# Kernel tuning notes

Measured on AMD Instinct MI355X. Metric: run time of the kernel, lower is better.

Reference implementation:

```python
import jax, jax.numpy as jnp
import numpy as np

D = 1024
DFF = 4096
B, S = 4, 2048
EPS = 1e-6
SLOPE = 0.01  # torch LeakyReLU default


def setup_inputs() -> dict:
    key = jax.random.key(0)
    ks = jax.random.split(key, 16)
    sd = 1.0 / np.sqrt(D)
    sf = 1.0 / np.sqrt(DFF)
    return {
        "X": jax.random.normal(ks[0], (B, S, D), dtype=jnp.float32),
        "intensity": jax.random.uniform(ks[1], (B, S, S), dtype=jnp.float32),
        "Wq": jax.random.uniform(ks[2], (D, D), jnp.float32, -sd, sd),
        "bq": jax.random.uniform(ks[3], (D,), jnp.float32, -sd, sd),
        "Wk": jax.random.uniform(ks[4], (D, D), jnp.float32, -sd, sd),
        "bk": jax.random.uniform(ks[5], (D,), jnp.float32, -sd, sd),
        "Wv": jax.random.uniform(ks[6], (D, D), jnp.float32, -sd, sd),
        "bv": jax.random.uniform(ks[7], (D,), jnp.float32, -sd, sd),
        "Wo": jax.random.uniform(ks[8], (D, D), jnp.float32, -sd, sd),
        "bo": jax.random.uniform(ks[9], (D,), jnp.float32, -sd, sd),
        "W1": jax.random.uniform(ks[10], (D, DFF), jnp.float32, -sd, sd),
        "b1": jax.random.uniform(ks[11], (DFF,), jnp.float32, -sd, sd),
        "W2": jax.random.uniform(ks[12], (DFF, D), jnp.float32, -sf, sf),
        "b2": jax.random.uniform(ks[13], (D,), jnp.float32, -sf, sf),
        "g1": jnp.ones((D,), jnp.float32),
        "be1": jnp.zeros((D,), jnp.float32),
        "g2": jnp.ones((D,), jnp.float32),
        "be2": jnp.zeros((D,), jnp.float32),
    }


def _layernorm(x, g, b):
    mu = jnp.mean(x, axis=-1, keepdims=True)
    var = jnp.mean(jnp.square(x - mu), axis=-1, keepdims=True)
    return (x - mu) * jax.lax.rsqrt(var + EPS) * g + b


def reference(X, intensity, Wq, bq, Wk, bk, Wv, bv, Wo, bo, W1, b1, W2, b2, g1, be1, g2, be2):
    d_k = X.shape[-1]
    q = X @ Wq + bq
    k = X @ Wk + bk
    v = X @ Wv + bv
    # scores: [B,S,S]; scale applied to k^T as in source
    scores = jnp.einsum('bid,bjd->bij', q, k) / jnp.sqrt(jnp.float32(d_k))
    attn = jax.nn.softmax(scores, axis=-1) + intensity  # post-softmax bias add
    out = jnp.einsum('bij,bjd->bid', attn, v) @ Wo + bo
    h = _layernorm(out + X, g1, be1)
    ffn = jax.nn.leaky_relu(h @ W1 + b1, negative_slope=SLOPE) @ W2 + b2
    return _layernorm(ffn + h, g2, be2)
```

## Files before the change

kernel.cpp:

```cpp
#include <hip/hip_runtime.h>

#define B_   4
#define S_   2048
#define D_   1024
#define DFF_ 4096

typedef __attribute__((ext_vector_type(8))) short short8;
typedef __attribute__((ext_vector_type(4))) float floatx4;

__device__ __forceinline__ unsigned short f2b(float f) {
    unsigned int u = __float_as_uint(f);
    unsigned int r = (u + 0x7fffu + ((u >> 16) & 1u)) >> 16;
    return (unsigned short)r;
}
__device__ __forceinline__ float b2f(unsigned short u) {
    return __uint_as_float((unsigned int)u << 16);
}

__device__ __forceinline__ void swizzle_xy(int gx, int gy, int& bx, int& by) {
    if ((gy & 7) == 0) {
        const int linear = by * gx + bx;
        const int xcd = linear & 7;
        const int slot = linear >> 3;
        const int r = slot / gx;
        by = xcd * (gy >> 3) + r;
        bx = slot - r * gx;
    }
}

__device__ __forceinline__ void gemm_core256(
    const unsigned short* __restrict__ A,
    const unsigned short* __restrict__ Bt,
    int ldA, int ldB, int K, int m0, int n0,
    unsigned short* As, unsigned short* Bs,
    floatx4 acc[4][4])
{
    const int tid  = threadIdx.x;
    const int lane = tid & 63;
    const int wave = tid >> 6;

    const int ra = tid >> 3;
    const int pg = tid & 7;
    const int cg = (pg ^ (ra & 7)) * 8;
    const unsigned short* gA = A  + (long long)(m0 + ra) * ldA + cg;
    const unsigned short* gB = Bt + (long long)(n0 + ra) * ldB + cg;
    const long long pA = 64LL * ldA;
    const long long pB = 64LL * ldB;

    unsigned short* dA = As + wave * 512;
    unsigned short* dB = Bs + wave * 512;

    const int wr = (wave >> 1) * 64;
    const int wc = (wave & 1) * 64;
    const int fr = lane & 15;
    const int q  = lane >> 4;

    int aoff[2][4], boff[2][4];
#pragma unroll
    for (int h = 0; h < 2; h++)
#pragma unroll
        for (int i = 0; i < 4; i++) {
            const int rA = wr + i * 16 + fr;
            const int rB = wc + i * 16 + fr;
            const int g  = h * 4 + q;
            aoff[h][i] = rA * 64 + ((g ^ (rA & 7)) * 8);
            boff[h][i] = rB * 64 + ((g ^ (rB & 7)) * 8);
        }

    for (int k0 = 0; k0 < K; k0 += 64) {
        __syncthreads();
#pragma unroll
        for (int p = 0; p < 4; p++)
            __builtin_amdgcn_global_load_lds(
                (const __attribute__((address_space(1))) void*)(gA + k0 + p * pA),
                (__attribute__((address_space(3))) void*)(dA + p * 4096), 16, 0, 0);
#pragma unroll
        for (int p = 0; p < 2; p++)
            __builtin_amdgcn_global_load_lds(
                (const __attribute__((address_space(1))) void*)(gB + k0 + p * pB),
                (__attribute__((address_space(3))) void*)(dB + p * 4096), 16, 0, 0);
        __syncthreads();

#pragma unroll
        for (int h = 0; h < 2; h++) {
            short8 af[4], bfr[4];
#pragma unroll
            for (int mi = 0; mi < 4; mi++) af[mi] = *(const short8*)&As[aoff[h][mi]];
#pragma unroll
            for (int ni = 0; ni < 4; ni++) bfr[ni] = *(const short8*)&Bs[boff[h][ni]];
#pragma unroll
            for (int mi = 0; mi < 4; mi++)
#pragma unroll
                for (int ni = 0; ni < 4; ni++)
                    acc[mi][ni] = __builtin_amdgcn_mfma_f32_16x16x32_bf16(
                        af[mi], bfr[ni], acc[mi][ni], 0, 0, 0);
        }
    }
}

__global__ __launch_bounds__(256) void cast_bf16_kernel(
    const float4* __restrict__ src, ushort4* __restrict__ dst, int n4)
{
    int i = blockIdx.x * 256 + threadIdx.x;
    if (i < n4) {
        float4 f = src[i];
        ushort4 u;
        u.x = f2b(f.x); u.y = f2b(f.y); u.z = f2b(f.z); u.w = f2b(f.w);
        dst[i] = u;
    }
}

__global__ __launch_bounds__(256) void transpose_cast_kernel(
    const float* __restrict__ W, unsigned short* __restrict__ Wt, int K, int N)
{
    __shared__ float tile[32][33];
    const int tx = threadIdx.x;
    const int ty = threadIdx.y;
    const int bx = blockIdx.x * 32;
    const int by = blockIdx.y * 32;
#pragma unroll
    for (int j = 0; j < 32; j += 8)
        tile[ty + j][tx] = W[(long long)(by + ty + j) * N + bx + tx];
    __syncthreads();
#pragma unroll
    for (int j = 0; j < 32; j += 8)
        Wt[(long long)(bx + ty + j) * K + by + tx] = f2b(tile[tx][ty + j]);
}

__global__ __launch_bounds__(256) void vtrans_kernel(
    const unsigned short* __restrict__ Vb, unsigned short* __restrict__ Vt)
{
    __shared__ unsigned short tile[64][68];
    const int b  = blockIdx.z;
    const int s0 = blockIdx.y * 64;
    const int d0 = blockIdx.x * 64;
    const int tx = threadIdx.x & 15;
    const int ty = threadIdx.x >> 4;

    const unsigned short* src = Vb + ((long long)b * S_ + s0) * D_ + d0;
#pragma unroll
    for (int j = 0; j < 4; j++) {
        const int s = j * 16 + ty;
        ushort4 v = *(const ushort4*)(src + (long long)s * D_ + tx * 4);
        tile[tx * 4 + 0][s] = v.x;
        tile[tx * 4 + 1][s] = v.y;
        tile[tx * 4 + 2][s] = v.z;
        tile[tx * 4 + 3][s] = v.w;
    }
    __syncthreads();
    unsigned short* dst = Vt + ((long long)b * D_ + d0) * S_ + s0;
#pragma unroll
    for (int j = 0; j < 4; j++) {
        const int d = j * 16 + ty;
        ushort4 v;
        v.x = tile[d][tx * 4 + 0];
        v.y = tile[d][tx * 4 + 1];
        v.z = tile[d][tx * 4 + 2];
        v.w = tile[d][tx * 4 + 3];
        *(ushort4*)(dst + (long long)d * S_ + tx * 4) = v;
    }
}

template <int OUT_BF16, int ACT_LEAKY, int HAS_BIAS>
__global__ __launch_bounds__(512, 4) void gemm_bt(
    const unsigned short* __restrict__ A,
    const unsigned short* __restrict__ Bt,
    void* __restrict__ Cptr,
    const float* __restrict__ bias,
    int M, int N, int K, float scale,
    long long sA, long long sB, long long sC)
{
    __shared__ unsigned short As[256 * 64];
    __shared__ unsigned short Bs[128 * 64];

    const int lane = threadIdx.x & 63;
    const int wave = threadIdx.x >> 6;
    const int z    = blockIdx.z;

    int bx = blockIdx.x, by = blockIdx.y;
    swizzle_xy(gridDim.x, gridDim.y, bx, by);
    const int m0 = by * 256;
    const int n0 = bx * 128;

    floatx4 acc[4][4];
#pragma unroll
    for (int i = 0; i < 4; i++)
#pragma unroll
        for (int j = 0; j < 4; j++) acc[i][j] = floatx4{0.f, 0.f, 0.f, 0.f};

    gemm_core256(A + (long long)z * sA, Bt + (long long)z * sB,
                 K, K, K, m0, n0, As, Bs, acc);

    const int wr = (wave >> 1) * 64;
    const int wc = (wave & 1) * 64;
    const int cr = (lane >> 4) * 4;
    const int cc = lane & 15;
    float* Cf = (float*)Cptr;
    unsigned short* Cb = (unsigned short*)Cptr;

#pragma unroll
    for (int mi = 0; mi < 4; mi++) {
#pragma unroll
        for (int ni = 0; ni < 4; ni++) {
            const int col = n0 + wc + ni * 16 + cc;
            const float bv = HAS_BIAS ? bias[col] : 0.0f;
#pragma unroll
            for (int r = 0; r < 4; r++) {
                const int row = m0 + wr + mi * 16 + cr + r;
                float v = acc[mi][ni][r] * scale + bv;
                if (ACT_LEAKY) v = (v > 0.0f) ? v : 0.01f * v;
                const long long idx = (long long)z * sC + (long long)row * N + col;
                if (OUT_BF16) Cb[idx] = f2b(v); else Cf[idx] = v;
            }
        }
    }
}

template <int NK>
__global__ __launch_bounds__(512, 4) void gemm_bt_sk(
    const unsigned short* __restrict__ A,
    const unsigned short* __restrict__ Bt,
    unsigned short* __restrict__ P,
    int M, int N, int Kslice, int ldA, int ldB,
    long long sA, long long sB)
{
    __shared__ unsigned short As[256 * 64];
    __shared__ unsigned short Bs[128 * 64];

    const int lane = threadIdx.x & 63;
    const int wave = threadIdx.x >> 6;
    const int z    = blockIdx.z;
    const int ks   = z % NK;
    const int b    = z / NK;
    const int nb   = gridDim.z / NK;

    int bx = blockIdx.x, by = blockIdx.y;
    swizzle_xy(gridDim.x, gridDim.y, bx, by);
    const int m0 = by * 256;
    const int n0 = bx * 128;

    floatx4 acc[4][4];
#pragma unroll
    for (int i = 0; i < 4; i++)
#pragma unroll
        for (int j = 0; j < 4; j++) acc[i][j] = floatx4{0.f, 0.f, 0.f, 0.f};

    gemm_core256(A + (long long)b * sA + (long long)ks * Kslice,
                 Bt + (long long)b * sB + (long long)ks * Kslice,
                 ldA, ldB, Kslice, m0, n0, As, Bs, acc);

    const long long pbase = ((long long)ks * nb + b) * (long long)M * N;

    const int wr = (wave >> 1) * 64;
    const int wc = (wave & 1) * 64;
    const int cr = (lane >> 4) * 4;
    const int cc = lane & 15;

#pragma unroll
    for (int mi = 0; mi < 4; mi++) {
#pragma unroll
        for (int ni = 0; ni < 4; ni++) {
            const int col = n0 + wc + ni * 16 + cc;
#pragma unroll
            for (int r = 0; r < 4; r++) {
                const int row = m0 + wr + mi * 16 + cr + r;
                P[pbase + (long long)row * N + col] = f2b(acc[mi][ni][r]);
            }
        }
    }
}

__global__ __launch_bounds__(512, 4) void gemm_qkv(
    const unsigned short* __restrict__ A,
    const unsigned short* __restrict__ Bt,
    unsigned short* __restrict__ Qb,
    unsigned short* __restrict__ Kb,
    unsigned short* __restrict__ Vb,
    const float* __restrict__ bq,
    const float* __restrict__ bk,
    const float* __restrict__ bv)
{
    __shared__ unsigned short As[256 * 64];
    __shared__ unsigned short Bs[128 * 64];

    const int lane = threadIdx.x & 63;
    const int wave = threadIdx.x >> 6;

    int bx = blockIdx.x, by = blockIdx.y;
    swizzle_xy(gridDim.x, gridDim.y, bx, by);
    const int m0 = by * 256;
    const int n0 = bx * 128;

    floatx4 acc[4][4];
#pragma unroll
    for (int i = 0; i < 4; i++)
#pragma unroll
        for (int j = 0; j < 4; j++) acc[i][j] = floatx4{0.f, 0.f, 0.f, 0.f};

    gemm_core256(A, Bt, D_, D_, D_, m0, n0, As, Bs, acc);

    const int wr = (wave >> 1) * 64;
    const int wc = (wave & 1) * 64;
    const int cr = (lane >> 4) * 4;
    const int cc = lane & 15;

#pragma unroll
    for (int mi = 0; mi < 4; mi++) {
#pragma unroll
        for (int ni = 0; ni < 4; ni++) {
            const int col = n0 + wc + ni * 16 + cc;
            const int seg = col >> 10;
            const int c = col & 1023;
            const float* bp = (seg == 0) ? bq : ((seg == 1) ? bk : bv);
            unsigned short* dp = (seg == 0) ? Qb : ((seg == 1) ? Kb : Vb);
            const float bval = bp[c];
#pragma unroll
            for (int r = 0; r < 4; r++) {
                const int row = m0 + wr + mi * 16 + cr + r;
                dp[(long long)row * D_ + c] = f2b(acc[mi][ni][r] + bval);
            }
        }
    }
}

__global__ __launch_bounds__(256) void avred_kernel(
    const ushort4* __restrict__ p0, const ushort4* __restrict__ p1,
    ushort4* __restrict__ dst, int n4)
{
    int i = blockIdx.x * 256 + threadIdx.x;
    if (i < n4) {
        ushort4 a = p0[i], b = p1[i];
        ushort4 u;
        u.x = f2b(b2f(a.x) + b2f(b.x)); u.y = f2b(b2f(a.y) + b2f(b.y));
        u.z = f2b(b2f(a.z) + b2f(b.z)); u.w = f2b(b2f(a.w) + b2f(b.w));
        dst[i] = u;
    }
}

template <int HAS_OUTB>
__global__ __launch_bounds__(256) void ln_red_kernel(
    const unsigned short* __restrict__ p0, const unsigned short* __restrict__ p1,
    const float* __restrict__ resid, const float* __restrict__ bias,
    const float* __restrict__ g, const float* __restrict__ b,
    float* __restrict__ out_f, unsigned short* __restrict__ out_b)
{
    __shared__ float red[8];
    const long long row = blockIdx.x;
    const int tid = threadIdx.x;
    const ushort4 a0 = ((const ushort4*)(p0 + row * D_))[tid];
    const ushort4 a1 = ((const ushort4*)(p1 + row * D_))[tid];
    const float4 rv = ((const float4*)(resid + row * D_))[tid];
    const float4 bi = ((const float4*)bias)[tid];
    float v0 = b2f(a0.x) + b2f(a1.x) + bi.x + rv.x;
    float v1 = b2f(a0.y) + b2f(a1.y) + bi.y + rv.y;
    float v2 = b2f(a0.z) + b2f(a1.z) + bi.z + rv.z;
    float v3 = b2f(a0.w) + b2f(a1.w) + bi.w + rv.w;

    float s = v0 + v1 + v2 + v3;
#pragma unroll
    for (int o = 32; o > 0; o >>= 1) s += __shfl_xor(s, o);
    if ((tid & 63) == 0) red[tid >> 6] = s;
    __syncthreads();
    const float mean = (red[0] + red[1] + red[2] + red[3]) * (1.0f / D_);

    const float d0 = v0 - mean, d1 = v1 - mean, d2 = v2 - mean, d3 = v3 - mean;
    float q = d0 * d0 + d1 * d1 + d2 * d2 + d3 * d3;
#pragma unroll
    for (int o = 32; o > 0; o >>= 1) q += __shfl_xor(q, o);
    if ((tid & 63) == 0) red[4 + (tid >> 6)] = q;
    __syncthreads();
    const float var = (red[4] + red[5] + red[6] + red[7]) * (1.0f / D_);
    const float inv = rsqrtf(var + 1e-6f);

    const float4 gv = ((const float4*)g)[tid];
    const float4 bv = ((const float4*)b)[tid];
    const float o0 = d0 * inv * gv.x + bv.x;
    const float o1 = d1 * inv * gv.y + bv.y;
    const float o2 = d2 * inv * gv.z + bv.z;
    const float o3 = d3 * inv * gv.w + bv.w;

    ((float4*)(out_f + row * D_))[tid] = float4{o0, o1, o2, o3};
    if (HAS_OUTB) {
        ushort4 u; u.x = f2b(o0); u.y = f2b(o1); u.z = f2b(o2); u.w = f2b(o3);
        ((ushort4*)(out_b + row * D_))[tid] = u;
    }
}

__global__ __launch_bounds__(256) void softmax_bias_kernel(
    const unsigned short* __restrict__ scores, const float* __restrict__ intensity,
    unsigned short* __restrict__ attn)
{
    __shared__ float red[8];
    const long long row = blockIdx.x;
    const int tid = threadIdx.x;
    const ushort4* s4 = (const ushort4*)(scores + row * S_);
    const float4* i4 = (const float4*)(intensity + row * S_);
    ushort4* dst = (ushort4*)(attn + row * S_);

    float vv[8];
    {
        ushort4 a = s4[tid], b = s4[tid + 256];
        vv[0] = b2f(a.x); vv[1] = b2f(a.y); vv[2] = b2f(a.z); vv[3] = b2f(a.w);
        vv[4] = b2f(b.x); vv[5] = b2f(b.y); vv[6] = b2f(b.z); vv[7] = b2f(b.w);
    }

    float mx = vv[0];
#pragma unroll
    for (int i = 1; i < 8; i++) mx = fmaxf(mx, vv[i]);
#pragma unroll
    for (int o = 32; o > 0; o >>= 1) mx = fmaxf(mx, __shfl_xor(mx, o));
    if ((tid & 63) == 0) red[tid >> 6] = mx;
    __syncthreads();
    mx = fmaxf(fmaxf(red[0], red[1]), fmaxf(red[2], red[3]));

    float e[8];
    float sum = 0.f;
#pragma unroll
    for (int i = 0; i < 8; i++) { e[i] = __expf(vv[i] - mx); sum += e[i]; }
#pragma unroll
    for (int o = 32; o > 0; o >>= 1) sum += __shfl_xor(sum, o);
    if ((tid & 63) == 0) red[4 + (tid >> 6)] = sum;
    __syncthreads();
    sum = red[4] + red[5] + red[6] + red[7];
    const float rs = 1.0f / sum;

#pragma unroll
    for (int i = 0; i < 2; i++) {
        float4 iv = i4[tid + 256 * i];
        ushort4 o;
        o.x = f2b(e[4 * i + 0] * rs + iv.x);
        o.y = f2b(e[4 * i + 1] * rs + iv.y);
        o.z = f2b(e[4 * i + 2] * rs + iv.z);
        o.w = f2b(e[4 * i + 3] * rs + iv.w);
        dst[tid + 256 * i] = o;
    }
}

extern "C" void kernel_launch(void* const* d_in, const int* in_sizes, int n_in,
                              void* d_out, int out_size, void* d_ws, size_t ws_size,
                              hipStream_t stream)
{
    const float* X   = (const float*)d_in[0];
    const float* inten = (const float*)d_in[1];
    const float* Wq  = (const float*)d_in[2];
    const float* bq  = (const float*)d_in[3];
    const float* Wk  = (const float*)d_in[4];
    const float* bk  = (const float*)d_in[5];
    const float* Wv  = (const float*)d_in[6];
    const float* bv  = (const float*)d_in[7];
    const float* Wo  = (const float*)d_in[8];
    const float* bo  = (const float*)d_in[9];
    const float* W1  = (const float*)d_in[10];
    const float* b1  = (const float*)d_in[11];
    const float* W2  = (const float*)d_in[12];
    const float* b2  = (const float*)d_in[13];
    const float* g1  = (const float*)d_in[14];
    const float* be1 = (const float*)d_in[15];
    const float* g2  = (const float*)d_in[16];
    const float* be2 = (const float*)d_in[17];
    float* out = (float*)d_out;

    char* ws = (char*)d_ws;
    const size_t MB = 1ull << 20;
    unsigned short* Xb   = (unsigned short*)(ws + 0);
    unsigned short* Wqkv = (unsigned short*)(ws + 16 * MB);
    unsigned short* Wot  = (unsigned short*)(ws + 22 * MB);
    unsigned short* W1t  = (unsigned short*)(ws + 24 * MB);
    unsigned short* W2t  = (unsigned short*)(ws + 32 * MB);
    unsigned short* Qb   = (unsigned short*)(ws + 40 * MB);
    unsigned short* Kb   = (unsigned short*)(ws + 56 * MB);
    unsigned short* Vt   = (unsigned short*)(ws + 72 * MB);
    unsigned short* Sc   = (unsigned short*)(ws + 88 * MB);
    unsigned short* Vb   = (unsigned short*)(ws + 152 * MB);
    unsigned short* At   = (unsigned short*)(ws + 152 * MB);
    unsigned short* AVp  = (unsigned short*)(ws + 88 * MB);
    unsigned short* AVb  = (unsigned short*)(ws + 0);
    unsigned short* Op   = (unsigned short*)(ws + 152 * MB);
    float*          Hf   = (float*)(ws + 40 * MB);
    unsigned short* Hb   = (unsigned short*)(ws + 72 * MB);
    unsigned short* F1   = (unsigned short*)(ws + 88 * MB);
    unsigned short* Fp   = (unsigned short*)(ws + 152 * MB);

    const dim3 blk(256);
    const dim3 blk512(512);
    const dim3 tblk(32, 8);
    const long long MN_d = (long long)B_ * S_ * D_;

    cast_bf16_kernel<<<dim3(8192), blk, 0, stream>>>(
        (const float4*)X, (ushort4*)Xb, B_ * S_ * D_ / 4);
    transpose_cast_kernel<<<dim3(D_ / 32, D_ / 32), tblk, 0, stream>>>(
        Wq, Wqkv, D_, D_);
    transpose_cast_kernel<<<dim3(D_ / 32, D_ / 32), tblk, 0, stream>>>(
        Wk, Wqkv + 1024 * 1024, D_, D_);
    transpose_cast_kernel<<<dim3(D_ / 32, D_ / 32), tblk, 0, stream>>>(
        Wv, Wqkv + 2048 * 1024, D_, D_);
    transpose_cast_kernel<<<dim3(D_ / 32, D_ / 32), tblk, 0, stream>>>(Wo, Wot, D_, D_);
    transpose_cast_kernel<<<dim3(DFF_ / 32, D_ / 32), tblk, 0, stream>>>(W1, W1t, D_, DFF_);
    transpose_cast_kernel<<<dim3(D_ / 32, DFF_ / 32), tblk, 0, stream>>>(W2, W2t, DFF_, D_);

    gemm_qkv<<<dim3(24, 32), blk512, 0, stream>>>(Xb, Wqkv, Qb, Kb, Vb, bq, bk, bv);

    vtrans_kernel<<<dim3(D_ / 64, S_ / 64, B_), blk, 0, stream>>>(Vb, Vt);

    gemm_bt<1, 0, 0><<<dim3(16, 8, 4), blk512, 0, stream>>>(
        Qb, Kb, Sc, nullptr, S_, S_, D_, 0.03125f,
        (long long)S_ * D_, (long long)S_ * D_, (long long)S_ * S_);

    softmax_bias_kernel<<<dim3(B_ * S_), blk, 0, stream>>>(Sc, inten, At);

    gemm_bt_sk<2><<<dim3(8, 8, 8), blk512, 0, stream>>>(
        At, Vt, AVp, S_, D_, S_ / 2, S_, S_,
        (long long)S_ * S_, (long long)D_ * S_);
    avred_kernel<<<dim3(8192), blk, 0, stream>>>(
        (const ushort4*)AVp, (const ushort4*)(AVp + MN_d), (ushort4*)AVb,
        (int)(MN_d / 4));

    gemm_bt_sk<2><<<dim3(8, 32, 2), blk512, 0, stream>>>(
        AVb, Wot, Op, B_ * S_, D_, D_ / 2, D_, D_, 0, 0);

    ln_red_kernel<1><<<dim3(B_ * S_), blk, 0, stream>>>(
        Op, Op + MN_d, X, bo, g1, be1, Hf, Hb);

    gemm_bt<1, 1, 1><<<dim3(32, 32), blk512, 0, stream>>>(
        Hb, W1t, F1, b1, B_ * S_, DFF_, D_, 1.0f, 0, 0, 0);

    gemm_bt_sk<2><<<dim3(8, 32, 2), blk512, 0, stream>>>(
        F1, W2t, Fp, B_ * S_, D_, DFF_ / 2, DFF_, DFF_, 0, 0);

    ln_red_kernel<0><<<dim3(B_ * S_), blk, 0, stream>>>(
        Fp, Fp + MN_d, Hf, b2, g2, be2, out, nullptr);
}
```

Measured before the change: 559.9 us.

## Use 256x256 double-buffered GEMM core with interleaved prefetch and MFMA

Replaces the 256x128 single-buffered GEMM mainloop with a 256x256 tile that double-buffers A and B in 128KB of LDS. Global-to-LDS loads for the next k-step are interleaved with fragment loads and MFMA quarter-blocks, using explicit vmcnt/lgkmcnt waits, barriers and setprio to keep the matrix cores busy. All GEMM launches get their grid halved along N, and launch bounds drop to 2 blocks per CU. The larger tile raises data reuse per block but gives fewer blocks, which risks wave-quantization and lower occupancy. The hand-tuned wait counts are fragile to get right.

```diff
diff --git a/kernel.cpp b/kernel.cpp
--- a/kernel.cpp
+++ b/kernel.cpp
@@ -28,74 +28,124 @@
     }
 }
 
-__device__ __forceinline__ void gemm_core256(
+#define GLL(src, dst) __builtin_amdgcn_global_load_lds( \
+    (const __attribute__((address_space(1))) void*)(src), \
+    (__attribute__((address_space(3))) void*)(dst), 16, 0, 0)
+
+__device__ __forceinline__ void barrier_mem() {
+    asm volatile("" ::: "memory");
+    __builtin_amdgcn_s_barrier();
+    asm volatile("" ::: "memory");
+}
+
+__device__ __forceinline__ void gemm_core256sq(
     const unsigned short* __restrict__ A,
     const unsigned short* __restrict__ Bt,
     int ldA, int ldB, int K, int m0, int n0,
-    unsigned short* As, unsigned short* Bs,
-    floatx4 acc[4][4])
+    unsigned short* __restrict__ lds,
+    floatx4 acc[8][4])
 {
     const int tid  = threadIdx.x;
     const int lane = tid & 63;
     const int wave = tid >> 6;
+    const int wm   = wave >> 2;
+    const int wn   = wave & 3;
 
     const int ra = tid >> 3;
     const int pg = tid & 7;
     const int cg = (pg ^ (ra & 7)) * 8;
     const unsigned short* gA = A  + (long long)(m0 + ra) * ldA + cg;
     const unsigned short* gB = Bt + (long long)(n0 + ra) * ldB + cg;
-    const long long pA = 64LL * ldA;
-    const long long pB = 64LL * ldB;
-
-    unsigned short* dA = As + wave * 512;
-    unsigned short* dB = Bs + wave * 512;
-
-    const int wr = (wave >> 1) * 64;
-    const int wc = (wave & 1) * 64;
+    const long long rsA = 64LL * ldA;
+    const long long rsB = 64LL * ldB;
+    unsigned short* const sAbase = lds + wave * 512;
+    unsigned short* const sBbase = lds + 32768 + wave * 512;
+
     const int fr = lane & 15;
     const int q  = lane >> 4;
-
-    int aoff[2][4], boff[2][4];
-#pragma unroll
-    for (int h = 0; h < 2; h++)
-#pragma unroll
-        for (int i = 0; i < 4; i++) {
-            const int rA = wr + i * 16 + fr;
-            const int rB = wc + i * 16 + fr;
-            const int g  = h * 4 + q;
-            aoff[h][i] = rA * 64 + ((g ^ (rA & 7)) * 8);
-            boff[h][i] = rB * 64 + ((g ^ (rB & 7)) * 8);
-        }
-
-    for (int k0 = 0; k0 < K; k0 += 64) {
-        __syncthreads();
-#pragma unroll
-        for (int p = 0; p < 4; p++)
-            __builtin_amdgcn_global_load_lds(
-                (const __attribute__((address_space(1))) void*)(gA + k0 + p * pA),
-                (__attribute__((address_space(3))) void*)(dA + p * 4096), 16, 0, 0);
-#pragma unroll
-        for (int p = 0; p < 2; p++)
-            __builtin_amdgcn_global_load_lds(
-                (const __attribute__((address_space(1))) void*)(gB + k0 + p * pB),
-                (__attribute__((address_space(3))) void*)(dB + p * 4096), 16, 0, 0);
-        __syncthreads();
-
-#pragma unroll
-        for (int h = 0; h < 2; h++) {
-            short8 af[4], bfr[4];
-#pragma unroll
-            for (int mi = 0; mi < 4; mi++) af[mi] = *(const short8*)&As[aoff[h][mi]];
-#pragma unroll
-            for (int ni = 0; ni < 4; ni++) bfr[ni] = *(const short8*)&Bs[boff[h][ni]];
-#pragma unroll
-            for (int mi = 0; mi < 4; mi++)
-#pragma unroll
-                for (int ni = 0; ni < 4; ni++)
-                    acc[mi][ni] = __builtin_amdgcn_mfma_f32_16x16x32_bf16(
-                        af[mi], bfr[ni], acc[mi][ni], 0, 0, 0);
-        }
-    }
+    const int sw0 = (q ^ (fr & 7)) * 8;
+    const int sw1 = sw0 ^ 32;
+    const unsigned short* const pA = lds + (wm * 128 + fr) * 64;
+    const unsigned short* const pB = lds + 32768 + (wn * 64 + fr) * 64;
+
+    short8 Af[4][2];
+    short8 Bf[2][2][2];
+
+#define STG_A(buf, h, kk) do { \
+    const unsigned short* _s = gA + (long long)(h) * 2 * rsA + (kk); \
+    unsigned short* _d = sAbase + (buf) * 16384 + (h) * 8192; \
+    GLL(_s, _d); GLL(_s + rsA, _d + 4096); } while (0)
+#define STG_B(buf, h, kk) do { \
+    const unsigned short* _s = gB + (long long)(h) * 2 * rsB + (kk); \
+    unsigned short* _d = sBbase + (buf) * 16384 + (h) * 8192; \
+    GLL(_s, _d); GLL(_s + rsB, _d + 4096); } while (0)
+#define LD_A(bufo, mh) do { \
+    _Pragma("unroll") for (int _i = 0; _i < 4; ++_i) { \
+        Af[_i][0] = *(const short8*)(pA + (bufo) + (mh) * 4096 + _i * 1024 + sw0); \
+        Af[_i][1] = *(const short8*)(pA + (bufo) + (mh) * 4096 + _i * 1024 + sw1); } } while (0)
+#define LD_B(bufo, np) do { \
+    _Pragma("unroll") for (int _j = 0; _j < 2; ++_j) { \
+        Bf[np][_j][0] = *(const short8*)(pB + (bufo) + (np) * 2048 + _j * 1024 + sw0); \
+        Bf[np][_j][1] = *(const short8*)(pB + (bufo) + (np) * 2048 + _j * 1024 + sw1); } } while (0)
+#define MM(mh, np) do { \
+    __builtin_amdgcn_s_setprio(1); \
+    _Pragma("unroll") for (int _i = 0; _i < 4; ++_i) \
+    _Pragma("unroll") for (int _j = 0; _j < 2; ++_j) \
+    _Pragma("unroll") for (int _h = 0; _h < 2; ++_h) \
+        acc[(mh) * 4 + _i][(np) * 2 + _j] = __builtin_amdgcn_mfma_f32_16x16x32_bf16( \
+            Af[_i][_h], Bf[np][_j][_h], acc[(mh) * 4 + _i][(np) * 2 + _j], 0, 0, 0); \
+    __builtin_amdgcn_s_setprio(0); } while (0)
+#define LGKM0() asm volatile("s_waitcnt lgkmcnt(0)" ::: "memory")
+#define VMC(n)  asm volatile("s_waitcnt vmcnt(" #n ")" ::: "memory")
+
+    const int NT = K >> 6;
+    const long long kcap = (long long)K - 64;
+
+    STG_B(0, 0, 0); STG_B(0, 1, 0);
+    STG_A(0, 0, 0); STG_A(0, 1, 0);
+    STG_B(1, 0, 64); STG_B(1, 1, 64);
+    VMC(4);
+    barrier_mem();
+
+    for (int t = 0; t < NT; t += 2) {
+        const long long k1 = (long long)(t + 1) * 64;
+        long long k2 = (long long)(t + 2) * 64; if (k2 > kcap) k2 = kcap;
+        long long k3 = (long long)(t + 3) * 64; if (k3 > kcap) k3 = kcap;
+
+        LD_A(0, 0); LD_B(0, 0);
+        STG_A(1, 0, k1);
+        barrier_mem(); LGKM0(); MM(0, 0); barrier_mem();
+        LD_B(0, 1);
+        STG_A(1, 1, k1);
+        barrier_mem(); LGKM0(); MM(0, 1); barrier_mem();
+        LD_A(0, 1);
+        STG_B(0, 0, k2);
+        barrier_mem(); LGKM0(); MM(1, 0); barrier_mem();
+        STG_B(0, 1, k2);
+        VMC(4);
+        barrier_mem(); MM(1, 1); barrier_mem();
+        LD_A(16384, 0); LD_B(16384, 0);
+        STG_A(0, 0, k2);
+        barrier_mem(); LGKM0(); MM(0, 0); barrier_mem();
+        LD_B(16384, 1);
+        STG_A(0, 1, k2);
+        barrier_mem(); LGKM0(); MM(0, 1); barrier_mem();
+        LD_A(16384, 1);
+        STG_B(1, 0, k3);
+        barrier_mem(); LGKM0(); MM(1, 0); barrier_mem();
+        STG_B(1, 1, k3);
+        VMC(4);
+        barrier_mem(); MM(1, 1); barrier_mem();
+    }
+    VMC(0);
+
+#undef STG_A
+#undef STG_B
+#undef LD_A
+#undef LD_B
+#undef MM
+#undef LGKM0
+#undef VMC
 }
 
 __global__ __launch_bounds__(256) void cast_bf16_kernel(
@@ -162,7 +212,7 @@
 }
 
 template <int OUT_BF16, int ACT_LEAKY, int HAS_BIAS>
-__global__ __launch_bounds__(512, 4) void gemm_bt(
+__global__ __launch_bounds__(512, 2) void gemm_bt(
     const unsigned short* __restrict__ A,
     const unsigned short* __restrict__ Bt,
     void* __restrict__ Cptr,
@@ -170,8 +220,7 @@
     int M, int N, int K, float scale,
     long long sA, long long sB, long long sC)
 {
-    __shared__ unsigned short As[256 * 64];
-    __shared__ unsigned short Bs[128 * 64];
+    __shared__ unsigned short lds[65536];
 
     const int lane = threadIdx.x & 63;
     const int wave = threadIdx.x >> 6;
@@ -180,26 +229,26 @@
     int bx = blockIdx.x, by = blockIdx.y;
     swizzle_xy(gridDim.x, gridDim.y, bx, by);
     const int m0 = by * 256;
-    const int n0 = bx * 128;
-
-    floatx4 acc[4][4];
-#pragma unroll
-    for (int i = 0; i < 4; i++)
+    const int n0 = bx * 256;
+
+    floatx4 acc[8][4];
+#pragma unroll
+    for (int i = 0; i < 8; i++)
 #pragma unroll
         for (int j = 0; j < 4; j++) acc[i][j] = floatx4{0.f, 0.f, 0.f, 0.f};
 
-    gemm_core256(A + (long long)z * sA, Bt + (long long)z * sB,
-                 K, K, K, m0, n0, As, Bs, acc);
-
-    const int wr = (wave >> 1) * 64;
-    const int wc = (wave & 1) * 64;
+    gemm_core256sq(A + (long long)z * sA, Bt + (long long)z * sB,
+                   K, K, K, m0, n0, lds, acc);
+
+    const int wr = (wave >> 2) * 128;
+    const int wc = (wave & 3) * 64;
     const int cr = (lane >> 4) * 4;
     const int cc = lane & 15;
     float* Cf = (float*)Cptr;
     unsigned short* Cb = (unsigned short*)Cptr;
 
 #pragma unroll
-    for (int mi = 0; mi < 4; mi++) {
+    for (int mi = 0; mi < 8; mi++) {
 #pragma unroll
         for (int ni = 0; ni < 4; ni++) {
             const int col = n0 + wc + ni * 16 + cc;
@@ -217,15 +266,14 @@
 }
 
 template <int NK>
-__global__ __launch_bounds__(512, 4) void gemm_bt_sk(
+__global__ __launch_bounds__(512, 2) void gemm_bt_sk(
     const unsigned short* __restrict__ A,
     const unsigned short* __restrict__ Bt,
     unsigned short* __restrict__ P,
     int M, int N, int Kslice, int ldA, int ldB,
     long long sA, long long sB)
 {
-    __shared__ unsigned short As[256 * 64];
-    __shared__ unsigned short Bs[128 * 64];
+    __shared__ unsigned short lds[65536];
 
     const int lane = threadIdx.x & 63;
     const int wave = threadIdx.x >> 6;
@@ -237,27 +285,27 @@
     int bx = blockIdx.x, by = blockIdx.y;
     swizzle_xy(gridDim.x, gridDim.y, bx, by);
     const int m0 = by * 256;
-    const int n0 = bx * 128;
-
-    floatx4 acc[4][4];
-#pragma unroll
-    for (int i = 0; i < 4; i++)
+    const int n0 = bx * 256;
+
+    floatx4 acc[8][4];
+#pragma unroll
+    for (int i = 0; i < 8; i++)
 #pragma unroll
         for (int j = 0; j < 4; j++) acc[i][j] = floatx4{0.f, 0.f, 0.f, 0.f};
 
-    gemm_core256(A + (long long)b * sA + (long long)ks * Kslice,
-                 Bt + (long long)b * sB + (long long)ks * Kslice,
-                 ldA, ldB, Kslice, m0, n0, As, Bs, acc);
+    gemm_core256sq(A + (long long)b * sA + (long long)ks * Kslice,
+                   Bt + (long long)b * sB + (long long)ks * Kslice,
+                   ldA, ldB, Kslice, m0, n0, lds, acc);
 
     const long long pbase = ((long long)ks * nb + b) * (long long)M * N;
 
-    const int wr = (wave >> 1) * 64;
-    const int wc = (wave & 1) * 64;
+    const int wr = (wave >> 2) * 128;
+    const int wc = (wave & 3) * 64;
     const int cr = (lane >> 4) * 4;
     const int cc = lane & 15;
 
 #pragma unroll
-    for (int mi = 0; mi < 4; mi++) {
+    for (int mi = 0; mi < 8; mi++) {
 #pragma unroll
         for (int ni = 0; ni < 4; ni++) {
             const int col = n0 + wc + ni * 16 + cc;
@@ -270,7 +318,7 @@
     }
 }
 
-__global__ __launch_bounds__(512, 4) void gemm_qkv(
+__global__ __launch_bounds__(512, 2) void gemm_qkv(
     const unsigned short* __restrict__ A,
     const unsigned short* __restrict__ Bt,
     unsigned short* __restrict__ Qb,
@@ -280,8 +328,7 @@
     const float* __restrict__ bk,
     const float* __restrict__ bv)
 {
-    __shared__ unsigned short As[256 * 64];
-    __shared__ unsigned short Bs[128 * 64];
+    __shared__ unsigned short lds[65536];
 
     const int lane = threadIdx.x & 63;
     const int wave = threadIdx.x >> 6;
@@ -289,23 +336,23 @@
     int bx = blockIdx.x, by = blockIdx.y;
     swizzle_xy(gridDim.x, gridDim.y, bx, by);
     const int m0 = by * 256;
-    const int n0 = bx * 128;
-
-    floatx4 acc[4][4];
-#pragma unroll
-    for (int i = 0; i < 4; i++)
+    const int n0 = bx * 256;
+
+    floatx4 acc[8][4];
+#pragma unroll
+    for (int i = 0; i < 8; i++)
 #pragma unroll
         for (int j = 0; j < 4; j++) acc[i][j] = floatx4{0.f, 0.f, 0.f, 0.f};
 
-    gemm_core256(A, Bt, D_, D_, D_, m0, n0, As, Bs, acc);
-
-    const int wr = (wave >> 1) * 64;
-    const int wc = (wave & 1) * 64;
+    gemm_core256sq(A, Bt, D_, D_, D_, m0, n0, lds, acc);
+
+    const int wr = (wave >> 2) * 128;
+    const int wc = (wave & 3) * 64;
     const int cr = (lane >> 4) * 4;
     const int cc = lane & 15;
 
 #pragma unroll
-    for (int mi = 0; mi < 4; mi++) {
+    for (int mi = 0; mi < 8; mi++) {
 #pragma unroll
         for (int ni = 0; ni < 4; ni++) {
             const int col = n0 + wc + ni * 16 + cc;
@@ -364,10 +411,10 @@
     const float mean = (red[0] + red[1] + red[2] + red[3]) * (1.0f / D_);
 
     const float d0 = v0 - mean, d1 = v1 - mean, d2 = v2 - mean, d3 = v3 - mean;
-    float q = d0 * d0 + d1 * d1 + d2 * d2 + d3 * d3;
-#pragma unroll
-    for (int o = 32; o > 0; o >>= 1) q += __shfl_xor(q, o);
-    if ((tid & 63) == 0) red[4 + (tid >> 6)] = q;
+    float qv = d0 * d0 + d1 * d1 + d2 * d2 + d3 * d3;
+#pragma unroll
+    for (int o = 32; o > 0; o >>= 1) qv += __shfl_xor(qv, o);
+    if ((tid & 63) == 0) red[4 + (tid >> 6)] = qv;
     __syncthreads();
     const float var = (red[4] + red[5] + red[6] + red[7]) * (1.0f / D_);
     const float inv = rsqrtf(var + 1e-6f);
@@ -498,33 +545,33 @@
     transpose_cast_kernel<<<dim3(DFF_ / 32, D_ / 32), tblk, 0, stream>>>(W1, W1t, D_, DFF_);
     transpose_cast_kernel<<<dim3(D_ / 32, DFF_ / 32), tblk, 0, stream>>>(W2, W2t, DFF_, D_);
 
-    gemm_qkv<<<dim3(24, 32), blk512, 0, stream>>>(Xb, Wqkv, Qb, Kb, Vb, bq, bk, bv);
+    gemm_qkv<<<dim3(12, 32), blk512, 0, stream>>>(Xb, Wqkv, Qb, Kb, Vb, bq, bk, bv);
 
     vtrans_kernel<<<dim3(D_ / 64, S_ / 64, B_), blk, 0, stream>>>(Vb, Vt);
 
-    gemm_bt<1, 0, 0><<<dim3(16, 8, 4), blk512, 0, stream>>>(
+    gemm_bt<1, 0, 0><<<dim3(8, 8, 4), blk512, 0, stream>>>(
         Qb, Kb, Sc, nullptr, S_, S_, D_, 0.03125f,
         (long long)S_ * D_, (long long)S_ * D_, (long long)S_ * S_);
 
     softmax_bias_kernel<<<dim3(B_ * S_), blk, 0, stream>>>(Sc, inten, At);
 
-    gemm_bt_sk<2><<<dim3(8, 8, 8), blk512, 0, stream>>>(
+    gemm_bt_sk<2><<<dim3(4, 8, 8), blk512, 0, stream>>>(
         At, Vt, AVp, S_, D_, S_ / 2, S_, S_,
         (long long)S_ * S_, (long long)D_ * S_);
     avred_kernel<<<dim3(8192), blk, 0, stream>>>(
         (const ushort4*)AVp, (const ushort4*)(AVp + MN_d), (ushort4*)AVb,
         (int)(MN_d / 4));
 
-    gemm_bt_sk<2><<<dim3(8, 32, 2), blk512, 0, stream>>>(
+    gemm_bt_sk<2><<<dim3(4, 32, 2), blk512, 0, stream>>>(
         AVb, Wot, Op, B_ * S_, D_, D_ / 2, D_, D_, 0, 0);
 
     ln_red_kernel<1><<<dim3(B_ * S_), blk, 0, stream>>>(
         Op, Op + MN_d, X, bo, g1, be1, Hf, Hb);
 
-    gemm_bt<1, 1, 1><<<dim3(32, 32), blk512, 0, stream>>>(
+    gemm_bt<1, 1, 1><<<dim3(16, 32), blk512, 0, stream>>>(
         Hb, W1t, F1, b1, B_ * S_, DFF_, D_, 1.0f, 0, 0, 0);
 
-    gemm_bt_sk<2><<<dim3(8, 32, 2), blk512, 0, stream>>>(
+    gemm_bt_sk<2><<<dim3(4, 32, 2), blk512, 0, stream>>>(
         F1, W2t, Fp, B_ * S_, D_, DFF_ / 2, DFF_, DFF_, 0, 0);
 
     ln_red_kernel<0><<<dim3(B_ * S_), blk, 0, stream>>>(
```

After: 545.3 us. -2.6%, faster.
